# Kernel optimization log

Hardware: AMD Instinct MI355X
Metric: run time of the kernel (lower is better)

## Reference

```python
import jax, jax.numpy as jnp
import numpy as np

N_ITER = 9      # n_iter in entmax_nsect_cuda(X, alpha=1.5, n_iter=9, n_sections=4)
N_SECTIONS = 4  # quaternary section search


def _entmax15_nsect(X):
    """1.5-entmax via n-section threshold search.

    p = [(alpha-1)*x - tau]_+^(1/(alpha-1)) with alpha=1.5 -> p = relu(x/2 - tau)^2,
    tau chosen so sum_j p_j = 1. tau lies in [max(x/2)-1, max(x/2)]; the interval is
    narrowed by N_SECTIONS-section search for N_ITER iterations (f is decreasing in tau).
    """
    Xs = X * 0.5
    mx = jnp.max(Xs, axis=-1, keepdims=True)      # (n, 1)
    lo = mx - 1.0
    hi = mx

    def f(tau):  # sum relu(x - tau)^2 - 1, decreasing in tau; (n, 1)
        return jnp.sum(jnp.square(jnp.maximum(Xs - tau, 0.0)), axis=-1, keepdims=True) - 1.0

    for _ in range(N_ITER):
        width = (hi - lo) / N_SECTIONS
        # count of interior grid points with f >= 0 gives the bracketing section index
        count = jnp.zeros_like(lo)
        for j in range(1, N_SECTIONS):
            count = count + (f(lo + j * width) >= 0.0).astype(Xs.dtype)
        lo = lo + width * count
        hi = lo + width

    tau = 0.5 * (lo + hi)
    p = jnp.square(jnp.maximum(Xs - tau, 0.0))
    return p / jnp.sum(p, axis=-1, keepdims=True)  # exact renormalization of approx projection


def setup_inputs() -> dict:
    key = jax.random.key(0)
    kx, kt = jax.random.split(key)
    n, c = 4096, 32000
    X = jax.random.normal(kx, (n, c), dtype=jnp.float32)
    target = jax.random.randint(kt, (n,), 0, c, dtype=jnp.int64)
    return {"X": X, "target": target}


def reference(X, target):
    n = X.shape[0]
    p = _entmax15_nsect(X)                                   # (n, C) simplex projection
    # omega (Tsallis entropy term for alpha=1.5): (1 - sum p^{1.5}) / 0.75
    omega = (1.0 - jnp.sum(p * jnp.sqrt(p), axis=-1)) / 0.75
    # p_star <- p - e_target  (scatter_add_ of -1 at the target column)
    p_star = p.at[jnp.arange(n), target].add(-1.0)
    loss = omega + jnp.sum(p_star * X, axis=-1)              # + einsum('ij,ij->i', p_star, X)
    # ignore_index = -100 < 0 -> no masking; reduction = 'elementwise_mean'
    return jnp.sum(loss) / n
```

## Files before the change

### kernel.cpp

```cpp
#include <hip/hip_runtime.h>


#define NTHR 1024
#define VPT4 8
#define CAP  8192
#define NITER 9

__global__ __launch_bounds__(NTHR, 8)
void entmax_row_kernel(const float* __restrict__ X,
                       const int* __restrict__ target,
                       float* __restrict__ row_loss,
                       int c) {
    const int r    = blockIdx.x;
    const int tid  = threadIdx.x;
    const int wave = tid >> 6;
    const int lane = tid & 63;
    const float* __restrict__ Xr = X + (size_t)r * (size_t)c;

    __shared__ float s_red[16];
    __shared__ float s_r3[3][16];
    __shared__ float s_bcast[4];
    __shared__ int   s_cnt;
    __shared__ float cand[CAP];

    const int c4 = c >> 2;

    float4 v[VPT4];
    #pragma unroll
    for (int k = 0; k < VPT4; ++k) {
        const int i4 = tid + k * NTHR;
        if (i4 < c4) {
            const float4 t4 = ((const float4*)Xr)[i4];
            v[k].x = 0.5f * t4.x; v[k].y = 0.5f * t4.y;
            v[k].z = 0.5f * t4.z; v[k].w = 0.5f * t4.w;
        } else {
            v[k].x = v[k].y = v[k].z = v[k].w = -1e30f;
        }
    }
    float tail = -1e30f;
    const int ti = (c4 << 2) + tid;
    if (ti < c) tail = 0.5f * Xr[ti];

    float m = tail;
    #pragma unroll
    for (int k = 0; k < VPT4; ++k)
        m = fmaxf(m, fmaxf(fmaxf(v[k].x, v[k].y), fmaxf(v[k].z, v[k].w)));
    #pragma unroll
    for (int off = 32; off > 0; off >>= 1)
        m = fmaxf(m, __shfl_xor(m, off));
    if (lane == 0) s_red[wave] = m;
    if (tid == 0) s_cnt = 0;
    __syncthreads();
    if (tid == 0) {
        float mm = s_red[0];
        for (int i = 1; i < 16; ++i) mm = fmaxf(mm, s_red[i]);
        s_bcast[0] = mm;
    }
    __syncthreads();
    const float mx = s_bcast[0];
    const float t0 = mx - 1.0f;

    int cnt = (tail > t0) ? 1 : 0;
    #pragma unroll
    for (int k = 0; k < VPT4; ++k)
        cnt += (v[k].x > t0) + (v[k].y > t0) + (v[k].z > t0) + (v[k].w > t0);
    int pos = 0;
    if (cnt > 0) pos = atomicAdd(&s_cnt, cnt);
    #pragma unroll
    for (int k = 0; k < VPT4; ++k) {
        if (v[k].x > t0) { if (pos < CAP) cand[pos] = v[k].x; ++pos; }
        if (v[k].y > t0) { if (pos < CAP) cand[pos] = v[k].y; ++pos; }
        if (v[k].z > t0) { if (pos < CAP) cand[pos] = v[k].z; ++pos; }
        if (v[k].w > t0) { if (pos < CAP) cand[pos] = v[k].w; ++pos; }
    }
    if (tail > t0) { if (pos < CAP) cand[pos] = tail; ++pos; }
    __syncthreads();
    const int total = s_cnt;

    if (total <= CAP) {
        if (wave == 0) {
            float lo = t0, hi = mx;
            for (int it = 0; it < NITER; ++it) {
                const float w  = (hi - lo) * 0.25f;
                const float t1 = lo + w, t2 = lo + 2.0f * w, t3 = lo + 3.0f * w;
                float f1 = 0.f, f2 = 0.f, f3 = 0.f;
                for (int i = lane; i < total; i += 64) {
                    const float x = cand[i];
                    const float d1 = fmaxf(x - t1, 0.f); f1 = fmaf(d1, d1, f1);
                    const float d2 = fmaxf(x - t2, 0.f); f2 = fmaf(d2, d2, f2);
                    const float d3 = fmaxf(x - t3, 0.f); f3 = fmaf(d3, d3, f3);
                }
                #pragma unroll
                for (int off = 32; off > 0; off >>= 1) {
                    f1 += __shfl_xor(f1, off);
                    f2 += __shfl_xor(f2, off);
                    f3 += __shfl_xor(f3, off);
                }
                const int cc = (f1 >= 1.f) + (f2 >= 1.f) + (f3 >= 1.f);
                lo = lo + w * (float)cc;
                hi = lo + w;
            }
            const float tau = 0.5f * (lo + hi);
            float S1 = 0.f, SX = 0.f, S3 = 0.f;
            for (int i = lane; i < total; i += 64) {
                const float x = cand[i];
                const float d = fmaxf(x - tau, 0.f);
                const float q = d * d;
                S1 += q;
                SX = fmaf(q, x, SX);
                S3 = fmaf(q, d, S3);
            }
            #pragma unroll
            for (int off = 32; off > 0; off >>= 1) {
                S1 += __shfl_xor(S1, off);
                SX += __shfl_xor(SX, off);
                S3 += __shfl_xor(S3, off);
            }
            if (lane == 0) {
                const float omega = (1.f - S3 / (S1 * sqrtf(S1))) * (4.f / 3.f);
                const int tg = target[r];
                row_loss[r] = omega + 2.f * SX / S1 - Xr[tg];
            }
        }
    } else {
        float lo = t0, hi = mx;
        for (int it = 0; it < NITER; ++it) {
            const float w  = (hi - lo) * 0.25f;
            const float t1 = lo + w, t2 = lo + 2.0f * w, t3 = lo + 3.0f * w;
            float f1 = 0.f, f2 = 0.f, f3 = 0.f;
            for (int i = tid; i < c; i += NTHR) {
                const float x = 0.5f * Xr[i];
                const float d1 = fmaxf(x - t1, 0.f); f1 = fmaf(d1, d1, f1);
                const float d2 = fmaxf(x - t2, 0.f); f2 = fmaf(d2, d2, f2);
                const float d3 = fmaxf(x - t3, 0.f); f3 = fmaf(d3, d3, f3);
            }
            #pragma unroll
            for (int off = 32; off > 0; off >>= 1) {
                f1 += __shfl_xor(f1, off);
                f2 += __shfl_xor(f2, off);
                f3 += __shfl_xor(f3, off);
            }
            if (lane == 0) { s_r3[0][wave] = f1; s_r3[1][wave] = f2; s_r3[2][wave] = f3; }
            __syncthreads();
            if (tid == 0) {
                float a = 0.f, b = 0.f, g = 0.f;
                for (int i = 0; i < 16; ++i) { a += s_r3[0][i]; b += s_r3[1][i]; g += s_r3[2][i]; }
                s_bcast[0] = a; s_bcast[1] = b; s_bcast[2] = g;
            }
            __syncthreads();
            const int cc = (s_bcast[0] >= 1.f) + (s_bcast[1] >= 1.f) + (s_bcast[2] >= 1.f);
            lo = lo + w * (float)cc;
            hi = lo + w;
        }
        const float tau = 0.5f * (lo + hi);
        float S1 = 0.f, SX = 0.f, S3 = 0.f;
        for (int i = tid; i < c; i += NTHR) {
            const float x = 0.5f * Xr[i];
            const float d = fmaxf(x - tau, 0.f);
            const float q = d * d;
            S1 += q; SX = fmaf(q, x, SX); S3 = fmaf(q, d, S3);
        }
        #pragma unroll
        for (int off = 32; off > 0; off >>= 1) {
            S1 += __shfl_xor(S1, off);
            SX += __shfl_xor(SX, off);
            S3 += __shfl_xor(S3, off);
        }
        if (lane == 0) { s_r3[0][wave] = S1; s_r3[1][wave] = SX; s_r3[2][wave] = S3; }
        __syncthreads();
        if (tid == 0) {
            float a = 0.f, b = 0.f, g = 0.f;
            for (int i = 0; i < 16; ++i) { a += s_r3[0][i]; b += s_r3[1][i]; g += s_r3[2][i]; }
            const float omega = (1.f - g / (a * sqrtf(a))) * (4.f / 3.f);
            const int tg = target[r];
            row_loss[r] = omega + 2.f * b / a - Xr[tg];
        }
    }
}

__global__ __launch_bounds__(NTHR)
void reduce_mean_kernel(const float* __restrict__ vv, float* __restrict__ out, int n) {
    __shared__ float s_red[16];
    float s = 0.f;
    for (int i = threadIdx.x; i < n; i += NTHR) s += vv[i];
    #pragma unroll
    for (int off = 32; off > 0; off >>= 1) s += __shfl_xor(s, off);
    const int wave = threadIdx.x >> 6;
    const int lane = threadIdx.x & 63;
    if (lane == 0) s_red[wave] = s;
    __syncthreads();
    if (threadIdx.x == 0) {
        float t = 0.f;
        for (int i = 0; i < 16; ++i) t += s_red[i];
        out[0] = t / (float)n;
    }
}

extern "C" void kernel_launch(void* const* d_in, const int* in_sizes, int n_in,
                              void* d_out, int out_size, void* d_ws, size_t ws_size,
                              hipStream_t stream) {
    const float* X      = (const float*)d_in[0];
    const int*   target = (const int*)d_in[1];
    float*       out    = (float*)d_out;
    float*       row_loss = (float*)d_ws;

    const int n = in_sizes[1];
    const int c = in_sizes[0] / n;

    entmax_row_kernel<<<n, NTHR, 0, stream>>>(X, target, row_loss, c);
    reduce_mean_kernel<<<1, NTHR, 0, stream>>>(row_loss, out, n);
}
```

Before: 173.3 us.

## Split rows into half-row blocks with global candidate buffers and separate search kernel

```diff
diff --git a/kernel.cpp b/kernel.cpp
--- a/kernel.cpp
+++ b/kernel.cpp
@@ -1,11 +1,187 @@
 #include <hip/hip_runtime.h>
 
 
-#define NTHR 1024
+#define NTHR   1024
+#define NITER  9
+#define SUBCAP 3072
+#define CAP    8192
+
+__global__ __launch_bounds__(NTHR, 8)
+void pass1_kernel(const float* __restrict__ X,
+                  float* __restrict__ maxes,
+                  int*   __restrict__ counts,
+                  float* __restrict__ cand,
+                  int c) {
+    const int sb   = blockIdx.x;
+    const int r    = sb >> 1;
+    const int h    = sb & 1;
+    const int tid  = threadIdx.x;
+    const int wave = tid >> 6;
+    const int lane = tid & 63;
+
+    const int half0 = c >> 1;
+    const int start = h ? half0 : 0;
+    const int len   = h ? (c - half0) : half0;
+    const float* __restrict__ Xh = X + (size_t)r * (size_t)c + start;
+
+    __shared__ float s_red[16];
+    __shared__ float s_b;
+    __shared__ int   s_cnt;
+
+    const int len4 = len >> 2;
+    float4 v[4];
+    #pragma unroll
+    for (int k = 0; k < 4; ++k) {
+        const int i4 = tid + k * NTHR;
+        if (i4 < len4) {
+            const float4 t = ((const float4*)Xh)[i4];
+            v[k].x = 0.5f * t.x; v[k].y = 0.5f * t.y;
+            v[k].z = 0.5f * t.z; v[k].w = 0.5f * t.w;
+        } else {
+            v[k].x = v[k].y = v[k].z = v[k].w = -1e30f;
+        }
+    }
+    float tail = -1e30f;
+    const int ti = (len4 << 2) + tid;
+    if (ti < len) tail = 0.5f * Xh[ti];
+
+    float m = tail;
+    #pragma unroll
+    for (int k = 0; k < 4; ++k)
+        m = fmaxf(m, fmaxf(fmaxf(v[k].x, v[k].y), fmaxf(v[k].z, v[k].w)));
+    #pragma unroll
+    for (int off = 32; off > 0; off >>= 1)
+        m = fmaxf(m, __shfl_xor(m, off));
+    if (lane == 0) s_red[wave] = m;
+    if (tid == 0) s_cnt = 0;
+    __syncthreads();
+    if (tid == 0) {
+        float mm = s_red[0];
+        for (int i = 1; i < 16; ++i) mm = fmaxf(mm, s_red[i]);
+        s_b = mm;
+        maxes[sb] = mm;
+    }
+    __syncthreads();
+    const float t0 = s_b - 1.0f;
+
+    int cnt = (tail > t0) ? 1 : 0;
+    #pragma unroll
+    for (int k = 0; k < 4; ++k)
+        cnt += (v[k].x > t0) + (v[k].y > t0) + (v[k].z > t0) + (v[k].w > t0);
+    int pos = 0;
+    if (cnt > 0) pos = atomicAdd(&s_cnt, cnt);
+    float* __restrict__ gc = cand + (size_t)sb * SUBCAP;
+    #pragma unroll
+    for (int k = 0; k < 4; ++k) {
+        if (v[k].x > t0) { if (pos < SUBCAP) gc[pos] = v[k].x; ++pos; }
+        if (v[k].y > t0) { if (pos < SUBCAP) gc[pos] = v[k].y; ++pos; }
+        if (v[k].z > t0) { if (pos < SUBCAP) gc[pos] = v[k].z; ++pos; }
+        if (v[k].w > t0) { if (pos < SUBCAP) gc[pos] = v[k].w; ++pos; }
+    }
+    if (tail > t0) { if (pos < SUBCAP) gc[pos] = tail; ++pos; }
+    __syncthreads();
+    if (tid == 0) counts[sb] = s_cnt;
+}
+
+__global__ __launch_bounds__(256, 4)
+void search_kernel(const float* __restrict__ X,
+                   const int*   __restrict__ target,
+                   const float* __restrict__ maxes,
+                   const int*   __restrict__ counts,
+                   const float* __restrict__ cand,
+                   float* __restrict__ row_loss,
+                   int n, int c) {
+    const int wave = threadIdx.x >> 6;
+    const int lane = threadIdx.x & 63;
+    const int r    = blockIdx.x * 4 + wave;
+    if (r >= n) return;
+
+    const float m0 = maxes[2 * r];
+    const float m1 = maxes[2 * r + 1];
+    const float mx = fmaxf(m0, m1);
+    const int   c0 = counts[2 * r];
+    const int   c1 = counts[2 * r + 1];
+    const float* __restrict__ g0 = cand + (size_t)(2 * r) * SUBCAP;
+    const float* __restrict__ g1 = cand + (size_t)(2 * r + 1) * SUBCAP;
+    const float* __restrict__ Xr = X + (size_t)r * (size_t)c;
+
+    float lo = mx - 1.0f, hi = mx;
+    float S1, SX, S3;
+
+    if (c0 <= SUBCAP && c1 <= SUBCAP) {
+        const int total = c0 + c1;
+        for (int it = 0; it < NITER; ++it) {
+            const float w  = (hi - lo) * 0.25f;
+            const float t1 = lo + w, t2 = lo + 2.0f * w, t3 = lo + 3.0f * w;
+            float f1 = 0.f, f2 = 0.f, f3 = 0.f;
+            for (int i = lane; i < total; i += 64) {
+                const float x = (i < c0) ? g0[i] : g1[i - c0];
+                const float d1 = fmaxf(x - t1, 0.f); f1 = fmaf(d1, d1, f1);
+                const float d2 = fmaxf(x - t2, 0.f); f2 = fmaf(d2, d2, f2);
+                const float d3 = fmaxf(x - t3, 0.f); f3 = fmaf(d3, d3, f3);
+            }
+            #pragma unroll
+            for (int off = 32; off > 0; off >>= 1) {
+                f1 += __shfl_xor(f1, off);
+                f2 += __shfl_xor(f2, off);
+                f3 += __shfl_xor(f3, off);
+            }
+            const int cc = (f1 >= 1.f) + (f2 >= 1.f) + (f3 >= 1.f);
+            lo = lo + w * (float)cc;
+            hi = lo + w;
+        }
+        const float tau = 0.5f * (lo + hi);
+        S1 = 0.f; SX = 0.f; S3 = 0.f;
+        for (int i = lane; i < total; i += 64) {
+            const float x = (i < c0) ? g0[i] : g1[i - c0];
+            const float d = fmaxf(x - tau, 0.f);
+            const float q = d * d;
+            S1 += q; SX = fmaf(q, x, SX); S3 = fmaf(q, d, S3);
+        }
+    } else {
+        for (int it = 0; it < NITER; ++it) {
+            const float w  = (hi - lo) * 0.25f;
+            const float t1 = lo + w, t2 = lo + 2.0f * w, t3 = lo + 3.0f * w;
+            float f1 = 0.f, f2 = 0.f, f3 = 0.f;
+            for (int i = lane; i < c; i += 64) {
+                const float x = 0.5f * Xr[i];
+                const float d1 = fmaxf(x - t1, 0.f); f1 = fmaf(d1, d1, f1);
+                const float d2 = fmaxf(x - t2, 0.f); f2 = fmaf(d2, d2, f2);
+                const float d3 = fmaxf(x - t3, 0.f); f3 = fmaf(d3, d3, f3);
+            }
+            #pragma unroll
+            for (int off = 32; off > 0; off >>= 1) {
+                f1 += __shfl_xor(f1, off);
+                f2 += __shfl_xor(f2, off);
+                f3 += __shfl_xor(f3, off);
+            }
+            const int cc = (f1 >= 1.f) + (f2 >= 1.f) + (f3 >= 1.f);
+            lo = lo + w * (float)cc;
+            hi = lo + w;
+        }
+        const float tau = 0.5f * (lo + hi);
+        S1 = 0.f; SX = 0.f; S3 = 0.f;
+        for (int i = lane; i < c; i += 64) {
+            const float x = 0.5f * Xr[i];
+            const float d = fmaxf(x - tau, 0.f);
+            const float q = d * d;
+            S1 += q; SX = fmaf(q, x, SX); S3 = fmaf(q, d, S3);
+        }
+    }
+    #pragma unroll
+    for (int off = 32; off > 0; off >>= 1) {
+        S1 += __shfl_xor(S1, off);
+        SX += __shfl_xor(SX, off);
+        S3 += __shfl_xor(S3, off);
+    }
+    if (lane == 0) {
+        const float omega = (1.f - S3 / (S1 * sqrtf(S1))) * (4.f / 3.f);
+        const int tg = target[r];
+        row_loss[r] = omega + 2.f * SX / S1 - Xr[tg];
+    }
+}
+
 #define VPT4 8
-#define CAP  8192
-#define NITER 9
-
 __global__ __launch_bounds__(NTHR, 8)
 void entmax_row_kernel(const float* __restrict__ X,
                        const int* __restrict__ target,
@@ -21,10 +197,9 @@
     __shared__ float s_r3[3][16];
     __shared__ float s_bcast[4];
     __shared__ int   s_cnt;
-    __shared__ float cand[CAP];
+    __shared__ float candl[CAP];
 
     const int c4 = c >> 2;
-
     float4 v[VPT4];
     #pragma unroll
     for (int k = 0; k < VPT4; ++k) {
@@ -68,12 +243,12 @@
     if (cnt > 0) pos = atomicAdd(&s_cnt, cnt);
     #pragma unroll
     for (int k = 0; k < VPT4; ++k) {
-        if (v[k].x > t0) { if (pos < CAP) cand[pos] = v[k].x; ++pos; }
-        if (v[k].y > t0) { if (pos < CAP) cand[pos] = v[k].y; ++pos; }
-        if (v[k].z > t0) { if (pos < CAP) cand[pos] = v[k].z; ++pos; }
-        if (v[k].w > t0) { if (pos < CAP) cand[pos] = v[k].w; ++pos; }
-    }
-    if (tail > t0) { if (pos < CAP) cand[pos] = tail; ++pos; }
+        if (v[k].x > t0) { if (pos < CAP) candl[pos] = v[k].x; ++pos; }
+        if (v[k].y > t0) { if (pos < CAP) candl[pos] = v[k].y; ++pos; }
+        if (v[k].z > t0) { if (pos < CAP) candl[pos] = v[k].z; ++pos; }
+        if (v[k].w > t0) { if (pos < CAP) candl[pos] = v[k].w; ++pos; }
+    }
+    if (tail > t0) { if (pos < CAP) candl[pos] = tail; ++pos; }
     __syncthreads();
     const int total = s_cnt;
 
@@ -85,7 +260,7 @@
                 const float t1 = lo + w, t2 = lo + 2.0f * w, t3 = lo + 3.0f * w;
                 float f1 = 0.f, f2 = 0.f, f3 = 0.f;
                 for (int i = lane; i < total; i += 64) {
-                    const float x = cand[i];
+                    const float x = candl[i];
                     const float d1 = fmaxf(x - t1, 0.f); f1 = fmaf(d1, d1, f1);
                     const float d2 = fmaxf(x - t2, 0.f); f2 = fmaf(d2, d2, f2);
                     const float d3 = fmaxf(x - t3, 0.f); f3 = fmaf(d3, d3, f3);
@@ -103,12 +278,10 @@
             const float tau = 0.5f * (lo + hi);
             float S1 = 0.f, SX = 0.f, S3 = 0.f;
             for (int i = lane; i < total; i += 64) {
-                const float x = cand[i];
+                const float x = candl[i];
                 const float d = fmaxf(x - tau, 0.f);
                 const float q = d * d;
-                S1 += q;
-                SX = fmaf(q, x, SX);
-                S3 = fmaf(q, d, S3);
+                S1 += q; SX = fmaf(q, x, SX); S3 = fmaf(q, d, S3);
             }
             #pragma unroll
             for (int off = 32; off > 0; off >>= 1) {
@@ -202,11 +375,23 @@
     const float* X      = (const float*)d_in[0];
     const int*   target = (const int*)d_in[1];
     float*       out    = (float*)d_out;
-    float*       row_loss = (float*)d_ws;
 
     const int n = in_sizes[1];
     const int c = in_sizes[0] / n;
 
-    entmax_row_kernel<<<n, NTHR, 0, stream>>>(X, target, row_loss, c);
+    char* ws = (char*)d_ws;
+    size_t off = 0;
+    float* row_loss = (float*)(ws + off); off += (((size_t)n * 4) + 255) & ~(size_t)255;
+    float* maxes    = (float*)(ws + off); off += (((size_t)2 * n * 4) + 255) & ~(size_t)255;
+    int*   counts   = (int*)  (ws + off); off += (((size_t)2 * n * 4) + 255) & ~(size_t)255;
+    float* cand     = (float*)(ws + off); off += (size_t)2 * n * SUBCAP * 4;
+
+    if (off <= ws_size && (c % 8) == 0) {
+        pass1_kernel<<<2 * n, NTHR, 0, stream>>>(X, maxes, counts, cand, c);
+        search_kernel<<<(n + 3) / 4, 256, 0, stream>>>(X, target, maxes, counts, cand,
+                                                       row_loss, n, c);
+    } else {
+        entmax_row_kernel<<<n, NTHR, 0, stream>>>(X, target, row_loss, c);
+    }
     reduce_mean_kernel<<<1, NTHR, 0, stream>>>(row_loss, out, n);
 }
```

After: 196.7 us. 1.13x slower.

## Split row processing into chunked candidate-filter pass and per-wave threshold search

Applied to the files above, without the earlier changes.

```diff
diff --git a/kernel.cpp b/kernel.cpp
--- a/kernel.cpp
+++ b/kernel.cpp
@@ -1,190 +1,204 @@
 #include <hip/hip_runtime.h>
 
 
-#define NTHR 1024
-#define VPT4 8
-#define CAP  8192
 #define NITER 9
-
-__global__ __launch_bounds__(NTHR, 8)
-void entmax_row_kernel(const float* __restrict__ X,
-                       const int* __restrict__ target,
-                       float* __restrict__ row_loss,
-                       int c) {
-    const int r    = blockIdx.x;
-    const int tid  = threadIdx.x;
-    const int wave = tid >> 6;
-    const int lane = tid & 63;
-    const float* __restrict__ Xr = X + (size_t)r * (size_t)c;
-
-    __shared__ float s_red[16];
-    __shared__ float s_r3[3][16];
-    __shared__ float s_bcast[4];
-    __shared__ int   s_cnt;
-    __shared__ float cand[CAP];
-
-    const int c4 = c >> 2;
-
+#define CHUNK 2048
+#define VPT4  8
+#define WCAP  1024
+#define RCAP  3072
+#define SW    4
+
+__device__ __forceinline__ float wave_max_f(float m) {
+    #pragma unroll
+    for (int off = 32; off > 0; off >>= 1) m = fmaxf(m, __shfl_xor(m, off));
+    return m;
+}
+__device__ __forceinline__ float wave_sum_f(float s) {
+    #pragma unroll
+    for (int off = 32; off > 0; off >>= 1) s += __shfl_xor(s, off);
+    return s;
+}
+
+__device__ float row_loss_fullscan(const float* __restrict__ Xr, int c,
+                                   int lane, int tg) {
+    float m = -3e38f;
+    for (int i = lane; i < c; i += 64) m = fmaxf(m, Xr[i]);
+    m = wave_max_f(m);
+    float lo = 0.5f * m - 1.0f, hi = 0.5f * m;
+    for (int it = 0; it < NITER; ++it) {
+        const float w  = (hi - lo) * 0.25f;
+        const float t1 = lo + w, t2 = lo + 2.0f * w, t3 = lo + 3.0f * w;
+        float f1 = 0.f, f2 = 0.f, f3 = 0.f;
+        for (int i = lane; i < c; i += 64) {
+            const float x = 0.5f * Xr[i];
+            float d;
+            d = fmaxf(x - t1, 0.f); f1 = fmaf(d, d, f1);
+            d = fmaxf(x - t2, 0.f); f2 = fmaf(d, d, f2);
+            d = fmaxf(x - t3, 0.f); f3 = fmaf(d, d, f3);
+        }
+        f1 = wave_sum_f(f1); f2 = wave_sum_f(f2); f3 = wave_sum_f(f3);
+        const int cc = (f1 >= 1.f) + (f2 >= 1.f) + (f3 >= 1.f);
+        lo += w * (float)cc;
+        hi = lo + w;
+    }
+    const float tau = 0.5f * (lo + hi);
+    float S1 = 0.f, SX = 0.f, S3 = 0.f;
+    for (int i = lane; i < c; i += 64) {
+        const float x = 0.5f * Xr[i];
+        const float d = fmaxf(x - tau, 0.f), q = d * d;
+        S1 += q; SX = fmaf(q, x, SX); S3 = fmaf(q, d, S3);
+    }
+    S1 = wave_sum_f(S1); SX = wave_sum_f(SX); S3 = wave_sum_f(S3);
+    const float omega = (1.f - S3 / (S1 * sqrtf(S1))) * (4.f / 3.f);
+    return omega + 2.f * SX / S1 - Xr[tg];
+}
+
+__global__ __launch_bounds__(256, 4)
+void pass1_kernel(const float* __restrict__ X,
+                  float* __restrict__ maxes,
+                  int*   __restrict__ counts,
+                  float* __restrict__ cand,
+                  int c, int cpr, int nchunks) {
+    const int wid  = blockIdx.x * 4 + (threadIdx.x >> 6);
+    const int lane = threadIdx.x & 63;
+    if (wid >= nchunks) return;
+    const int r    = wid / cpr;
+    const int ch   = wid - r * cpr;
+    const int base = ch * CHUNK;
+    const int len  = min(CHUNK, c - base);
+    const float* __restrict__ Xc = X + (size_t)r * (size_t)c + base;
+
+    const int len4 = len >> 2;
     float4 v[VPT4];
     #pragma unroll
     for (int k = 0; k < VPT4; ++k) {
-        const int i4 = tid + k * NTHR;
-        if (i4 < c4) {
-            const float4 t4 = ((const float4*)Xr)[i4];
-            v[k].x = 0.5f * t4.x; v[k].y = 0.5f * t4.y;
-            v[k].z = 0.5f * t4.z; v[k].w = 0.5f * t4.w;
-        } else {
-            v[k].x = v[k].y = v[k].z = v[k].w = -1e30f;
-        }
-    }
-    float tail = -1e30f;
-    const int ti = (c4 << 2) + tid;
-    if (ti < c) tail = 0.5f * Xr[ti];
-
-    float m = tail;
+        const int i4 = lane + (k << 6);
+        if (i4 < len4) v[k] = ((const float4*)Xc)[i4];
+        else { v[k].x = v[k].y = v[k].z = v[k].w = -3e38f; }
+    }
+
+    float m = -3e38f;
     #pragma unroll
     for (int k = 0; k < VPT4; ++k)
         m = fmaxf(m, fmaxf(fmaxf(v[k].x, v[k].y), fmaxf(v[k].z, v[k].w)));
-    #pragma unroll
-    for (int off = 32; off > 0; off >>= 1)
-        m = fmaxf(m, __shfl_xor(m, off));
-    if (lane == 0) s_red[wave] = m;
-    if (tid == 0) s_cnt = 0;
-    __syncthreads();
-    if (tid == 0) {
-        float mm = s_red[0];
-        for (int i = 1; i < 16; ++i) mm = fmaxf(mm, s_red[i]);
-        s_bcast[0] = mm;
-    }
-    __syncthreads();
-    const float mx = s_bcast[0];
-    const float t0 = mx - 1.0f;
-
-    int cnt = (tail > t0) ? 1 : 0;
-    #pragma unroll
-    for (int k = 0; k < VPT4; ++k)
-        cnt += (v[k].x > t0) + (v[k].y > t0) + (v[k].z > t0) + (v[k].w > t0);
-    int pos = 0;
-    if (cnt > 0) pos = atomicAdd(&s_cnt, cnt);
+    m = wave_max_f(m);
+    const float t0 = m - 2.0f;
+
+    float* __restrict__ slot = cand + (size_t)wid * WCAP;
+    const unsigned long long lt = (((unsigned long long)1) << lane) - 1ull;
+    int total = 0;
     #pragma unroll
     for (int k = 0; k < VPT4; ++k) {
-        if (v[k].x > t0) { if (pos < CAP) cand[pos] = v[k].x; ++pos; }
-        if (v[k].y > t0) { if (pos < CAP) cand[pos] = v[k].y; ++pos; }
-        if (v[k].z > t0) { if (pos < CAP) cand[pos] = v[k].z; ++pos; }
-        if (v[k].w > t0) { if (pos < CAP) cand[pos] = v[k].w; ++pos; }
-    }
-    if (tail > t0) { if (pos < CAP) cand[pos] = tail; ++pos; }
-    __syncthreads();
-    const int total = s_cnt;
-
-    if (total <= CAP) {
-        if (wave == 0) {
-            float lo = t0, hi = mx;
-            for (int it = 0; it < NITER; ++it) {
-                const float w  = (hi - lo) * 0.25f;
-                const float t1 = lo + w, t2 = lo + 2.0f * w, t3 = lo + 3.0f * w;
-                float f1 = 0.f, f2 = 0.f, f3 = 0.f;
-                for (int i = lane; i < total; i += 64) {
-                    const float x = cand[i];
-                    const float d1 = fmaxf(x - t1, 0.f); f1 = fmaf(d1, d1, f1);
-                    const float d2 = fmaxf(x - t2, 0.f); f2 = fmaf(d2, d2, f2);
-                    const float d3 = fmaxf(x - t3, 0.f); f3 = fmaf(d3, d3, f3);
-                }
-                #pragma unroll
-                for (int off = 32; off > 0; off >>= 1) {
-                    f1 += __shfl_xor(f1, off);
-                    f2 += __shfl_xor(f2, off);
-                    f3 += __shfl_xor(f3, off);
-                }
-                const int cc = (f1 >= 1.f) + (f2 >= 1.f) + (f3 >= 1.f);
-                lo = lo + w * (float)cc;
-                hi = lo + w;
+        const float e[4] = {v[k].x, v[k].y, v[k].z, v[k].w};
+        #pragma unroll
+        for (int j = 0; j < 4; ++j) {
+            const bool p = e[j] > t0;
+            const unsigned long long b = __ballot(p);
+            const int pos = total + __popcll(b & lt);
+            if (p && pos < WCAP) slot[pos] = e[j];
+            total += (int)__popcll(b);
+        }
+    }
+    if (lane == 0) { maxes[wid] = m; counts[wid] = total; }
+}
+
+__global__ __launch_bounds__(256, 2)
+void search_kernel(const float* __restrict__ X,
+                   const int*   __restrict__ target,
+                   const float* __restrict__ maxes,
+                   const int*   __restrict__ counts,
+                   const float* __restrict__ cand,
+                   float* __restrict__ row_loss,
+                   int n, int c, int cpr) {
+    __shared__ float lds[SW][RCAP];
+    const int wave = threadIdx.x >> 6;
+    const int lane = threadIdx.x & 63;
+    const int r    = blockIdx.x * SW + wave;
+    if (r >= n) return;
+    float* __restrict__ rb = lds[wave];
+    const float* __restrict__ Xr = X + (size_t)r * (size_t)c;
+    const int tg = target[r];
+
+    float m = (lane < cpr) ? maxes[r * cpr + lane] : -3e38f;
+    m = wave_max_f(m);
+    const float t0 = m - 2.0f;
+
+    bool ovf = (lane < cpr) ? (counts[r * cpr + lane] > WCAP) : false;
+    ovf = __any(ovf);
+
+    int cnt = 0;
+    if (!ovf) {
+        const unsigned long long lt = (((unsigned long long)1) << lane) - 1ull;
+        for (int chn = 0; chn < cpr; ++chn) {
+            const int cc = counts[r * cpr + chn];
+            const float* __restrict__ sl = cand + (size_t)(r * cpr + chn) * WCAP;
+            for (int i0 = 0; i0 < cc; i0 += 64) {
+                const int  i  = i0 + lane;
+                const bool vl = i < cc;
+                const float x = vl ? sl[i] : -3e38f;
+                const bool p  = vl && (x > t0);
+                const unsigned long long b = __ballot(p);
+                const int pos = cnt + (int)__popcll(b & lt);
+                if (p && pos < RCAP) rb[pos] = 0.5f * x;
+                cnt += (int)__popcll(b);
             }
-            const float tau = 0.5f * (lo + hi);
-            float S1 = 0.f, SX = 0.f, S3 = 0.f;
-            for (int i = lane; i < total; i += 64) {
-                const float x = cand[i];
-                const float d = fmaxf(x - tau, 0.f);
-                const float q = d * d;
-                S1 += q;
-                SX = fmaf(q, x, SX);
-                S3 = fmaf(q, d, S3);
-            }
-            #pragma unroll
-            for (int off = 32; off > 0; off >>= 1) {
-                S1 += __shfl_xor(S1, off);
-                SX += __shfl_xor(SX, off);
-                S3 += __shfl_xor(S3, off);
-            }
-            if (lane == 0) {
-                const float omega = (1.f - S3 / (S1 * sqrtf(S1))) * (4.f / 3.f);
-                const int tg = target[r];
-                row_loss[r] = omega + 2.f * SX / S1 - Xr[tg];
-            }
-        }
-    } else {
-        float lo = t0, hi = mx;
+        }
+        if (cnt > RCAP) ovf = true;
+    }
+
+    float loss;
+    if (!ovf) {
+        float lo = 0.5f * m - 1.0f, hi = 0.5f * m;
         for (int it = 0; it < NITER; ++it) {
             const float w  = (hi - lo) * 0.25f;
             const float t1 = lo + w, t2 = lo + 2.0f * w, t3 = lo + 3.0f * w;
             float f1 = 0.f, f2 = 0.f, f3 = 0.f;
-            for (int i = tid; i < c; i += NTHR) {
-                const float x = 0.5f * Xr[i];
-                const float d1 = fmaxf(x - t1, 0.f); f1 = fmaf(d1, d1, f1);
-                const float d2 = fmaxf(x - t2, 0.f); f2 = fmaf(d2, d2, f2);
-                const float d3 = fmaxf(x - t3, 0.f); f3 = fmaf(d3, d3, f3);
+            for (int i = lane; i < cnt; i += 64) {
+                const float x = rb[i];
+                float d;
+                d = fmaxf(x - t1, 0.f); f1 = fmaf(d, d, f1);
+                d = fmaxf(x - t2, 0.f); f2 = fmaf(d, d, f2);
+                d = fmaxf(x - t3, 0.f); f3 = fmaf(d, d, f3);
             }
-            #pragma unroll
-            for (int off = 32; off > 0; off >>= 1) {
-                f1 += __shfl_xor(f1, off);
-                f2 += __shfl_xor(f2, off);
-                f3 += __shfl_xor(f3, off);
-            }
-            if (lane == 0) { s_r3[0][wave] = f1; s_r3[1][wave] = f2; s_r3[2][wave] = f3; }
-            __syncthreads();
-            if (tid == 0) {
-                float a = 0.f, b = 0.f, g = 0.f;
-                for (int i = 0; i < 16; ++i) { a += s_r3[0][i]; b += s_r3[1][i]; g += s_r3[2][i]; }
-                s_bcast[0] = a; s_bcast[1] = b; s_bcast[2] = g;
-            }
-            __syncthreads();
-            const int cc = (s_bcast[0] >= 1.f) + (s_bcast[1] >= 1.f) + (s_bcast[2] >= 1.f);
-            lo = lo + w * (float)cc;
+            f1 = wave_sum_f(f1); f2 = wave_sum_f(f2); f3 = wave_sum_f(f3);
+            const int cc = (f1 >= 1.f) + (f2 >= 1.f) + (f3 >= 1.f);
+            lo += w * (float)cc;
             hi = lo + w;
         }
         const float tau = 0.5f * (lo + hi);
         float S1 = 0.f, SX = 0.f, S3 = 0.f;
-        for (int i = tid; i < c; i += NTHR) {
-            const float x = 0.5f * Xr[i];
-            const float d = fmaxf(x - tau, 0.f);
-            const float q = d * d;
+        for (int i = lane; i < cnt; i += 64) {
+            const float x = rb[i];
+            const float d = fmaxf(x - tau, 0.f), q = d * d;
             S1 += q; SX = fmaf(q, x, SX); S3 = fmaf(q, d, S3);
         }
-        #pragma unroll
-        for (int off = 32; off > 0; off >>= 1) {
-            S1 += __shfl_xor(S1, off);
-            SX += __shfl_xor(SX, off);
-            S3 += __shfl_xor(S3, off);
-        }
-        if (lane == 0) { s_r3[0][wave] = S1; s_r3[1][wave] = SX; s_r3[2][wave] = S3; }
-        __syncthreads();
-        if (tid == 0) {
-            float a = 0.f, b = 0.f, g = 0.f;
-            for (int i = 0; i < 16; ++i) { a += s_r3[0][i]; b += s_r3[1][i]; g += s_r3[2][i]; }
-            const float omega = (1.f - g / (a * sqrtf(a))) * (4.f / 3.f);
-            const int tg = target[r];
-            row_loss[r] = omega + 2.f * b / a - Xr[tg];
-        }
-    }
-}
-
-__global__ __launch_bounds__(NTHR)
+        S1 = wave_sum_f(S1); SX = wave_sum_f(SX); S3 = wave_sum_f(S3);
+        const float omega = (1.f - S3 / (S1 * sqrtf(S1))) * (4.f / 3.f);
+        loss = omega + 2.f * SX / S1 - Xr[tg];
+    } else {
+        loss = row_loss_fullscan(Xr, c, lane, tg);
+    }
+    if (lane == 0) row_loss[r] = loss;
+}
+
+__global__ __launch_bounds__(256, 4)
+void fallback_kernel(const float* __restrict__ X, const int* __restrict__ target,
+                     float* __restrict__ row_loss, int n, int c) {
+    const int wave = threadIdx.x >> 6;
+    const int lane = threadIdx.x & 63;
+    const int r = blockIdx.x * 4 + wave;
+    if (r >= n) return;
+    const float* __restrict__ Xr = X + (size_t)r * (size_t)c;
+    const float L = row_loss_fullscan(Xr, c, lane, target[r]);
+    if (lane == 0) row_loss[r] = L;
+}
+
+__global__ __launch_bounds__(1024)
 void reduce_mean_kernel(const float* __restrict__ vv, float* __restrict__ out, int n) {
     __shared__ float s_red[16];
     float s = 0.f;
-    for (int i = threadIdx.x; i < n; i += NTHR) s += vv[i];
-    #pragma unroll
-    for (int off = 32; off > 0; off >>= 1) s += __shfl_xor(s, off);
+    for (int i = threadIdx.x; i < n; i += 1024) s += vv[i];
+    s = wave_sum_f(s);
     const int wave = threadIdx.x >> 6;
     const int lane = threadIdx.x & 63;
     if (lane == 0) s_red[wave] = s;
@@ -202,11 +216,30 @@
     const float* X      = (const float*)d_in[0];
     const int*   target = (const int*)d_in[1];
     float*       out    = (float*)d_out;
-    float*       row_loss = (float*)d_ws;
-
-    const int n = in_sizes[1];
-    const int c = in_sizes[0] / n;
-
-    entmax_row_kernel<<<n, NTHR, 0, stream>>>(X, target, row_loss, c);
-    reduce_mean_kernel<<<1, NTHR, 0, stream>>>(row_loss, out, n);
-}
+
+    const int n   = in_sizes[1];
+    const int c   = in_sizes[0] / n;
+    const int cpr = (c + CHUNK - 1) / CHUNK;
+    const long long nchunks = (long long)n * cpr;
+
+    char* ws = (char*)d_ws;
+    size_t off = 0;
+    float* row_loss = (float*)(ws + off); off += (((size_t)n * 4) + 255) & ~(size_t)255;
+    float* maxes    = (float*)(ws + off); off += (((size_t)nchunks * 4) + 255) & ~(size_t)255;
+    int*   counts   = (int*)  (ws + off); off += (((size_t)nchunks * 4) + 255) & ~(size_t)255;
+    float* cand     = (float*)(ws + off); off += (size_t)nchunks * WCAP * 4;
+
+    const bool fast = (off <= ws_size) && ((c & 3) == 0) && (cpr <= 64) &&
+                      (nchunks < (1ll << 31));
+
+    if (fast) {
+        const int p1_blocks = (int)((nchunks + 3) / 4);
+        pass1_kernel<<<p1_blocks, 256, 0, stream>>>(X, maxes, counts, cand,
+                                                    c, cpr, (int)nchunks);
+        search_kernel<<<(n + SW - 1) / SW, 256, 0, stream>>>(X, target, maxes, counts,
+                                                             cand, row_loss, n, c, cpr);
+    } else {
+        fallback_kernel<<<(n + 3) / 4, 256, 0, stream>>>(X, target, row_loss, n, c);
+    }
+    reduce_mean_kernel<<<1, 1024, 0, stream>>>(row_loss, out, n);
+}
```

Result: slower. 214.1 us (+23.6%).
